# Optimization experiments

Measured on AMD Instinct MI355X. Metric: run time of the kernel, lower is better.

Reference implementation:

```python
import jax, jax.numpy as jnp
import numpy as np

N, E, F_IN, H, L, G, NH, HD, C = 50000, 640000, 64, 128, 3, 64, 8, 16, 2


def setup_inputs() -> dict:
    key = jax.random.key(0)
    k = jax.random.split(key, 12)
    s = 0.02
    return {
        "x": jax.random.normal(k[0], (N, F_IN), jnp.float32),
        "edge_index": jax.random.randint(k[1], (2, E), 0, N),
        "batch_idx": jnp.sort(jax.random.randint(k[2], (N,), 0, G)),
        "emb_w": jax.random.normal(k[3], (H, F_IN), jnp.float32) * s,
        "emb_b": jnp.zeros((H,), jnp.float32),
        "gcn_w": jax.random.normal(k[4], (L, H, H), jnp.float32) * s,
        "gcn_b": jnp.zeros((L, H), jnp.float32),
        "lstm_w_ih": jax.random.normal(k[5], (4 * H, H), jnp.float32) * s,
        "lstm_w_hh": jax.random.normal(k[6], (4 * H, H), jnp.float32) * s,
        "lstm_b_ih": jnp.zeros((4 * H,), jnp.float32),
        "lstm_b_hh": jnp.zeros((4 * H,), jnp.float32),
        "attn_in_w": jax.random.normal(k[7], (3 * H, H), jnp.float32) * s,
        "attn_in_b": jnp.zeros((3 * H,), jnp.float32),
        "attn_out_w": jax.random.normal(k[8], (H, H), jnp.float32) * s,
        "attn_out_b": jnp.zeros((H,), jnp.float32),
        "cls_w1": jax.random.normal(k[9], (H // 2, H), jnp.float32) * s,
        "cls_b1": jnp.zeros((H // 2,), jnp.float32),
        "cls_w2": jax.random.normal(k[10], (C, H // 2), jnp.float32) * s,
        "cls_b2": jnp.zeros((C,), jnp.float32),
    }


def reference(x, edge_index, batch_idx, emb_w, emb_b, gcn_w, gcn_b,
              lstm_w_ih, lstm_w_hh, lstm_b_ih, lstm_b_hh,
              attn_in_w, attn_in_b, attn_out_w, attn_out_b,
              cls_w1, cls_b1, cls_w2, cls_b2):
    src, dst = edge_index[0], edge_index[1]
    # GCN symmetric norm with self-loops (PyG gcn_norm): deg includes the self loop
    deg = jax.ops.segment_sum(jnp.ones((E,), x.dtype), dst, num_segments=N) + 1.0
    dis = jax.lax.rsqrt(deg)                      # deg^{-1/2}, deg >= 1
    norm = dis[src] * dis[dst]                    # [E]
    self_norm = dis * dis                         # [N], self-loop weight

    h = x @ emb_w.T + emb_b                       # node embedding [N, H]
    for l in range(L):
        hw = h @ gcn_w[l].T                       # linear transform [N, H]
        agg = jax.ops.segment_sum(hw[src] * norm[:, None], dst, num_segments=N)
        agg = agg + hw * self_norm[:, None]       # self-loop contribution
        h = jax.nn.relu(agg + gcn_b[l])

    # global mean pool per graph
    sums = jax.ops.segment_sum(h, batch_idx, num_segments=G)
    counts = jax.ops.segment_sum(jnp.ones((N,), h.dtype), batch_idx, num_segments=G)
    ge = sums / jnp.maximum(counts, 1.0)[:, None]  # [G, H]

    # LSTM with seq_len=1, h0=c0=0 (W_hh term vanishes); gate order i,f,g,o
    gates = ge @ lstm_w_ih.T + lstm_b_ih + lstm_b_hh
    i, f, g, o = jnp.split(gates, 4, axis=-1)
    c = jax.nn.sigmoid(i) * jnp.tanh(g)
    hs = jax.nn.sigmoid(o) * jnp.tanh(c)           # [G, H]

    # MultiheadAttention, seq_len=1 self-attention
    q, kk, v = jnp.split(hs @ attn_in_w.T + attn_in_b, 3, axis=-1)
    qh = q.reshape(G, NH, HD)
    kh = kk.reshape(G, NH, HD)
    vh = v.reshape(G, NH, HD)
    scores = jnp.einsum('bhd,bhd->bh', qh, kh) / jnp.sqrt(jnp.asarray(HD, hs.dtype))
    attn = jax.nn.softmax(scores[..., None], axis=-1)[..., 0]  # single key -> all ones
    ctx = (attn[..., None] * vh).reshape(G, H)
    fe = ctx @ attn_out_w.T + attn_out_b           # attended_out.mean(dim=1) with S=1

    # classifier (dropout is identity at inference)
    z = jax.nn.relu(fe @ cls_w1.T + cls_b1)
    return z @ cls_w2.T + cls_b2
```

## Files before the change

### kernel.cpp

```cpp
#include <hip/hip_runtime.h>
#include <math.h>

#define N_NODES 50000
#define N_EDGES 640000
#define F_INDIM 64
#define HDIM 128
#define NLAYERS 3
#define NGRAPH 64
#define NCLS 2
#define SCAN_BLOCKS ((N_NODES + 255) / 256)
#define POOL_SPLIT 8
#define NTILES (N_NODES / 16)

typedef __attribute__((ext_vector_type(8))) short bf16x8;
typedef __attribute__((ext_vector_type(4))) float f32x4;

__device__ __forceinline__ float bf_lo(unsigned v) { return __uint_as_float(v << 16); }
__device__ __forceinline__ float bf_hi(unsigned v) { return __uint_as_float(v & 0xffff0000u); }
__device__ __forceinline__ unsigned short f2bf(float f) {
    unsigned b = __float_as_uint(f);
    return (unsigned short)((b + 0x7fffu + ((b >> 16) & 1u)) >> 16);
}


__global__ __launch_bounds__(256) void k_init(int* cnt) {
    int i = blockIdx.x * 256 + threadIdx.x;
    if (i < N_NODES) cnt[i] = 0;
}

__global__ __launch_bounds__(256) void k_rank(const int* __restrict__ dst,
                                              int* __restrict__ cnt,
                                              int* __restrict__ rank) {
    int e = blockIdx.x * 256 + threadIdx.x;
    if (e < N_EDGES) rank[e] = atomicAdd(&cnt[dst[e]], 1);
}

__global__ __launch_bounds__(256) void k_scan1(const int* __restrict__ hist,
                                               int* __restrict__ row_start,
                                               int* __restrict__ partials,
                                               float* __restrict__ dis) {
    __shared__ int buf[256];
    int i = blockIdx.x * 256 + threadIdx.x;
    int v = (i < N_NODES) ? hist[i] : 0;
    if (i < N_NODES) dis[i] = rsqrtf((float)v + 1.0f);
    buf[threadIdx.x] = v;
    __syncthreads();
#pragma unroll
    for (int off = 1; off < 256; off <<= 1) {
        int t = (threadIdx.x >= off) ? buf[threadIdx.x - off] : 0;
        __syncthreads();
        buf[threadIdx.x] += t;
        __syncthreads();
    }
    if (i < N_NODES) row_start[i] = buf[threadIdx.x] - v;
    if (threadIdx.x == 255) partials[blockIdx.x] = buf[255];
}

__global__ __launch_bounds__(256) void k_scan2(int* __restrict__ partials) {
    __shared__ int buf[256];
    int v = (threadIdx.x < SCAN_BLOCKS) ? partials[threadIdx.x] : 0;
    buf[threadIdx.x] = v;
    __syncthreads();
#pragma unroll
    for (int off = 1; off < 256; off <<= 1) {
        int t = (threadIdx.x >= off) ? buf[threadIdx.x - off] : 0;
        __syncthreads();
        buf[threadIdx.x] += t;
        __syncthreads();
    }
    if (threadIdx.x < SCAN_BLOCKS) partials[threadIdx.x] = buf[threadIdx.x] - v;
}

__global__ __launch_bounds__(256) void k_scan3(int* __restrict__ row_start,
                                               const int* __restrict__ partials) {
    int i = blockIdx.x * 256 + threadIdx.x;
    if (i < N_NODES) row_start[i] += partials[blockIdx.x];
    if (i == 0) row_start[N_NODES] = N_EDGES;
}

#define PLACE_BLOCKS ((N_EDGES + 255) / 256)
#define CVT_Q1 (N_NODES * F_INDIM / 4)
#define CVT_Q2 (CVT_Q1 + HDIM * F_INDIM / 4)
#define CVT_Q3 (CVT_Q2 + NLAYERS * HDIM * HDIM / 4)
#define CVT_BLOCKS ((CVT_Q3 + 255) / 256)
#define ZERO_N (NGRAPH * HDIM + NGRAPH)
#define ZERO_BLOCKS ((ZERO_N + 255) / 256)

__global__ __launch_bounds__(256) void k_prep(const int* __restrict__ src,
                                              const int* __restrict__ dst,
                                              const int* __restrict__ rank,
                                              const float* __restrict__ dis,
                                              const int* __restrict__ row_start,
                                              uint2* __restrict__ csr,
                                              const float* __restrict__ x,
                                              const float* __restrict__ emb_w,
                                              const float* __restrict__ gcn_w,
                                              unsigned short* __restrict__ dst0,
                                              float* __restrict__ pool_counts) {
    int b = blockIdx.x;
    if (b < PLACE_BLOCKS) {
        int e = b * 256 + threadIdx.x;
        if (e >= N_EDGES) return;
        int s = src[e], d = dst[e];
        uint2 rec;
        rec.x = (unsigned)s;
        rec.y = __float_as_uint(dis[s] * dis[d]);
        csr[row_start[d] + rank[e]] = rec;
    } else if (b < PLACE_BLOCKS + CVT_BLOCKS) {
        int i = (b - PLACE_BLOCKS) * 256 + threadIdx.x;
        if (i >= CVT_Q3) return;
        const float* s;
        int off;
        if (i < CVT_Q1)      { s = x;     off = i; }
        else if (i < CVT_Q2) { s = emb_w; off = i - CVT_Q1; }
        else                 { s = gcn_w; off = i - CVT_Q2; }
        float4 v = *(const float4*)&s[off * 4];
        unsigned r0 = (unsigned)f2bf(v.x) | ((unsigned)f2bf(v.y) << 16);
        unsigned r1 = (unsigned)f2bf(v.z) | ((unsigned)f2bf(v.w) << 16);
        *(uint2*)&dst0[i * 4] = make_uint2(r0, r1);
    } else {
        int i = (b - PLACE_BLOCKS - CVT_BLOCKS) * 256 + threadIdx.x;
        if (i < ZERO_N) pool_counts[i] = 0.f;
    }
}


template<int K>
__global__ __launch_bounds__(256) void k_mm(const unsigned short* __restrict__ A,
                                            const unsigned short* __restrict__ W,
                                            const float* __restrict__ bias,
                                            unsigned short* __restrict__ C) {
    constexpr int KS = K / 32;
    int lane = threadIdx.x & 63;
    int lg = lane >> 4, lr = lane & 15;
    int cb = (threadIdx.x >> 6) * 32;
    int tile0 = blockIdx.x * 4;

    bf16x8 wf[2][KS];
#pragma unroll
    for (int ct = 0; ct < 2; ++ct)
#pragma unroll
        for (int ks = 0; ks < KS; ++ks)
            wf[ct][ks] = *(const bf16x8*)&W[(size_t)(cb + ct * 16 + lr) * K + ks * 32 + lg * 8];

    float b0 = bias ? bias[cb + lr] : 0.f;
    float b1 = bias ? bias[cb + 16 + lr] : 0.f;

    int ntile = NTILES - tile0; if (ntile > 4) ntile = 4;
    for (int t = 0; t < ntile; ++t) {
        int rb = (tile0 + t) * 16;
        f32x4 acc0 = {0.f, 0.f, 0.f, 0.f}, acc1 = {0.f, 0.f, 0.f, 0.f};
#pragma unroll
        for (int ks = 0; ks < KS; ++ks) {
            bf16x8 af = *(const bf16x8*)&A[(size_t)(rb + lr) * K + ks * 32 + lg * 8];
            acc0 = __builtin_amdgcn_mfma_f32_16x16x32_bf16(af, wf[0][ks], acc0, 0, 0, 0);
            acc1 = __builtin_amdgcn_mfma_f32_16x16x32_bf16(af, wf[1][ks], acc1, 0, 0, 0);
        }
        int row = rb + lg * 4;
#pragma unroll
        for (int j = 0; j < 4; ++j) {
            C[(size_t)(row + j) * HDIM + cb + lr]      = f2bf(acc0[j] + b0);
            C[(size_t)(row + j) * HDIM + cb + 16 + lr] = f2bf(acc1[j] + b1);
        }
    }
}


__global__ __launch_bounds__(256) void k_gather(const unsigned short* __restrict__ hw,
                                                const int* __restrict__ row_start,
                                                const uint2* __restrict__ csr,
                                                const float* __restrict__ dis,
                                                const float* __restrict__ bias,
                                                unsigned short* __restrict__ hout) {
    int n = blockIdx.x * 4 + (threadIdx.x >> 6);
    int lane = threadIdx.x & 63;
    int half = lane >> 5;
    int cl = lane & 31;
    int beg = row_start[n], end = row_start[n + 1];
    float a0 = 0.f, a1 = 0.f, a2 = 0.f, a3 = 0.f;
    for (int e = beg; e < end; e += 16) {
        unsigned sidx[8]; float w[8]; uint2 v[8];
#pragma unroll
        for (int u = 0; u < 8; ++u) {
            int me = e + 2 * u + half;
            uint2 rec = csr[min(me, end - 1)];
            sidx[u] = rec.x;
            w[u] = (me < end) ? __uint_as_float(rec.y) : 0.f;
        }
#pragma unroll
        for (int u = 0; u < 8; ++u)
            v[u] = *(const uint2*)&hw[(size_t)sidx[u] * HDIM + cl * 4];
#pragma unroll
        for (int u = 0; u < 8; ++u) {
            a0 += w[u] * bf_lo(v[u].x);
            a1 += w[u] * bf_hi(v[u].x);
            a2 += w[u] * bf_lo(v[u].y);
            a3 += w[u] * bf_hi(v[u].y);
        }
    }
    a0 += __shfl_xor(a0, 32); a1 += __shfl_xor(a1, 32);
    a2 += __shfl_xor(a2, 32); a3 += __shfl_xor(a3, 32);
    if (half == 0) {
        float dn = dis[n], sn = dn * dn;
        uint2 vs = *(const uint2*)&hw[(size_t)n * HDIM + cl * 4];
        a0 += sn * bf_lo(vs.x); a1 += sn * bf_hi(vs.x);
        a2 += sn * bf_lo(vs.y); a3 += sn * bf_hi(vs.y);
        float4 b = *(const float4*)&bias[cl * 4];
        a0 = fmaxf(a0 + b.x, 0.f); a1 = fmaxf(a1 + b.y, 0.f);
        a2 = fmaxf(a2 + b.z, 0.f); a3 = fmaxf(a3 + b.w, 0.f);
        uint2 r;
        r.x = (unsigned)f2bf(a0) | ((unsigned)f2bf(a1) << 16);
        r.y = (unsigned)f2bf(a2) | ((unsigned)f2bf(a3) << 16);
        *(uint2*)&hout[(size_t)n * HDIM + cl * 4] = r;
    }
}


__global__ __launch_bounds__(256) void k_pool(const unsigned short* __restrict__ h,
                                              const int* __restrict__ batch,
                                              float* __restrict__ pool,
                                              float* __restrict__ counts) {
    int g  = blockIdx.x >> 3;
    int sp = blockIdx.x & 7;
    int s, e;
    {
        int lo = 0, hi = N_NODES;
        while (lo < hi) { int mid = (lo + hi) >> 1; if (batch[mid] < g) lo = mid + 1; else hi = mid; }
        s = lo;
        lo = s; hi = N_NODES;
        while (lo < hi) { int mid = (lo + hi) >> 1; if (batch[mid] < g + 1) lo = mid + 1; else hi = mid; }
        e = lo;
    }
    int len = e - s;
    int chunk = (len + POOL_SPLIT - 1) / POOL_SPLIT;
    int ss = s + sp * chunk;
    int ee = min(ss + chunk, e);
    int cp = threadIdx.x & 63;
    int r  = threadIdx.x >> 6;
    float a0 = 0.f, a1 = 0.f;
    for (int n = ss + r; n < ee; n += 4) {
        unsigned v = *(const unsigned*)&h[(size_t)n * HDIM + cp * 2];
        a0 += bf_lo(v);
        a1 += bf_hi(v);
    }
    __shared__ float red0[4][64], red1[4][64];
    red0[r][cp] = a0; red1[r][cp] = a1;
    __syncthreads();
    if (r == 0) {
#pragma unroll
        for (int j = 1; j < 4; ++j) { a0 += red0[j][cp]; a1 += red1[j][cp]; }
        atomicAdd(&pool[g * HDIM + cp * 2], a0);
        atomicAdd(&pool[g * HDIM + cp * 2 + 1], a1);
    }
    if (threadIdx.x == 0 && ee > ss) atomicAdd(&counts[g], (float)(ee - ss));
}


__global__ __launch_bounds__(128) void k_tail(const float* __restrict__ pool,
                                              const float* __restrict__ counts,
                                              const float* __restrict__ w_ih,
                                              const float* __restrict__ b_ih,
                                              const float* __restrict__ b_hh,
                                              const float* __restrict__ attn_in_w,
                                              const float* __restrict__ attn_in_b,
                                              const float* __restrict__ attn_out_w,
                                              const float* __restrict__ attn_out_b,
                                              const float* __restrict__ w1,
                                              const float* __restrict__ b1,
                                              const float* __restrict__ w2,
                                              const float* __restrict__ b2,
                                              float* __restrict__ out) {
    __shared__ float ge[128], hsr[128], vv[128], fe[128], zz[64];
    int g = blockIdx.x, t = threadIdx.x;
    float cnt = fmaxf(counts[g], 1.0f);
    ge[t] = pool[g * HDIM + t] / cnt;
    __syncthreads();
    float gi = 0.f, gg = 0.f, go = 0.f;
    for (int k = 0; k < 128; ++k) {
        float xv = ge[k];
        gi += xv * w_ih[t * HDIM + k];
        gg += xv * w_ih[(256 + t) * HDIM + k];
        go += xv * w_ih[(384 + t) * HDIM + k];
    }
    gi += b_ih[t] + b_hh[t];
    gg += b_ih[256 + t] + b_hh[256 + t];
    go += b_ih[384 + t] + b_hh[384 + t];
    float cc = (1.f / (1.f + expf(-gi))) * tanhf(gg);
    float hv = (1.f / (1.f + expf(-go))) * tanhf(cc);
    hsr[t] = hv;
    __syncthreads();
    float va = attn_in_b[256 + t];
    for (int k = 0; k < 128; ++k) va += hsr[k] * attn_in_w[(256 + t) * HDIM + k];
    vv[t] = va;
    __syncthreads();
    float fv = attn_out_b[t];
    for (int k = 0; k < 128; ++k) fv += vv[k] * attn_out_w[t * HDIM + k];
    fe[t] = fv;
    __syncthreads();
    if (t < 64) {
        float zv = b1[t];
        for (int k = 0; k < 128; ++k) zv += fe[k] * w1[t * HDIM + k];
        zz[t] = fmaxf(zv, 0.f);
    }
    __syncthreads();
    if (t < NCLS) {
        float ov = b2[t];
        for (int k = 0; k < 64; ++k) ov += zz[k] * w2[t * 64 + k];
        out[g * NCLS + t] = ov;
    }
}


extern "C" void kernel_launch(void* const* d_in, const int* in_sizes, int n_in,
                              void* d_out, int out_size, void* d_ws, size_t ws_size,
                              hipStream_t stream) {
    const float* x          = (const float*)d_in[0];
    const int*   edge_index = (const int*)d_in[1];
    const int*   batch      = (const int*)d_in[2];
    const float* emb_w      = (const float*)d_in[3];
    const float* emb_b      = (const float*)d_in[4];
    const float* gcn_w      = (const float*)d_in[5];
    const float* gcn_b      = (const float*)d_in[6];
    const float* w_ih       = (const float*)d_in[7];
    const float* b_ih       = (const float*)d_in[9];
    const float* b_hh       = (const float*)d_in[10];
    const float* attn_in_w  = (const float*)d_in[11];
    const float* attn_in_b  = (const float*)d_in[12];
    const float* attn_out_w = (const float*)d_in[13];
    const float* attn_out_b = (const float*)d_in[14];
    const float* w1         = (const float*)d_in[15];
    const float* b1         = (const float*)d_in[16];
    const float* w2         = (const float*)d_in[17];
    const float* b2         = (const float*)d_in[18];
    float* out = (float*)d_out;

    int*   iws = (int*)d_ws;
    float* fws = (float*)d_ws;
    int*   cnt       = iws;
    float* dis       = fws + N_NODES;
    int*   row_start = iws + 2 * N_NODES;
    int*   rank      = iws + 3 * N_NODES + 4;
    uint2* csr       = (uint2*)(iws + 3 * N_NODES + 4 + N_EDGES);
    unsigned short* bws   = (unsigned short*)(iws + 3 * N_NODES + 4 + N_EDGES + 2 * N_EDGES);
    unsigned short* x_bf  = bws;
    unsigned short* we_bf = x_bf + (size_t)N_NODES * F_INDIM;
    unsigned short* wg_bf = we_bf + HDIM * F_INDIM;
    unsigned short* hA    = wg_bf + NLAYERS * HDIM * HDIM;
    unsigned short* hB    = hA + (size_t)N_NODES * HDIM;
    float* pool     = (float*)(hB + (size_t)N_NODES * HDIM);
    float* counts   = pool + NGRAPH * HDIM;
    int*   partials = (int*)(counts + NGRAPH);

    const int* src = edge_index;
    const int* dst = edge_index + N_EDGES;

    k_init<<<196, 256, 0, stream>>>(cnt);
    k_rank<<<(N_EDGES + 255) / 256, 256, 0, stream>>>(dst, cnt, rank);
    k_scan1<<<SCAN_BLOCKS, 256, 0, stream>>>(cnt, row_start, partials, dis);
    k_scan2<<<1, 256, 0, stream>>>(partials);
    k_scan3<<<SCAN_BLOCKS, 256, 0, stream>>>(row_start, partials);

    k_prep<<<PLACE_BLOCKS + CVT_BLOCKS + ZERO_BLOCKS, 256, 0, stream>>>(
        src, dst, rank, dis, row_start, csr, x, emb_w, gcn_w, x_bf, pool);

    int mm_grid = (NTILES + 3) / 4;
    k_mm<F_INDIM><<<mm_grid, 256, 0, stream>>>(x_bf, we_bf, emb_b, hA);
    for (int l = 0; l < NLAYERS; ++l) {
        k_mm<HDIM><<<mm_grid, 256, 0, stream>>>(hA, wg_bf + l * HDIM * HDIM, nullptr, hB);
        k_gather<<<N_NODES / 4, 256, 0, stream>>>(hB, row_start, csr, dis,
                                                  gcn_b + l * HDIM, hA);
    }
    k_pool<<<NGRAPH * POOL_SPLIT, 256, 0, stream>>>(hA, batch, pool, counts);
    k_tail<<<NGRAPH, 128, 0, stream>>>(pool, counts, w_ih, b_ih, b_hh,
                                       attn_in_w, attn_in_b, attn_out_w, attn_out_b,
                                       w1, b1, w2, b2, out);
}
```

Measured before the change: 261.1 us.

## Build CSR via bucketed two-pass sort and drop per-edge norm weights

```diff
diff --git a/kernel.cpp b/kernel.cpp
--- a/kernel.cpp
+++ b/kernel.cpp
@@ -8,9 +8,12 @@
 #define NLAYERS 3
 #define NGRAPH 64
 #define NCLS 2
-#define SCAN_BLOCKS ((N_NODES + 255) / 256)
 #define POOL_SPLIT 8
 #define NTILES (N_NODES / 16)
+
+#define NBUCK 64
+#define BNODES 782
+#define BSTRIDE 12288
 
 typedef __attribute__((ext_vector_type(8))) short bf16x8;
 typedef __attribute__((ext_vector_type(4))) float f32x4;
@@ -23,62 +26,133 @@
 }
 
 
-__global__ __launch_bounds__(256) void k_init(int* cnt) {
-    int i = blockIdx.x * 256 + threadIdx.x;
-    if (i < N_NODES) cnt[i] = 0;
-}
-
-__global__ __launch_bounds__(256) void k_rank(const int* __restrict__ dst,
-                                              int* __restrict__ cnt,
-                                              int* __restrict__ rank) {
-    int e = blockIdx.x * 256 + threadIdx.x;
-    if (e < N_EDGES) rank[e] = atomicAdd(&cnt[dst[e]], 1);
-}
-
-__global__ __launch_bounds__(256) void k_scan1(const int* __restrict__ hist,
+__global__ __launch_bounds__(256) void k_init(int* bcursor) {
+    if (threadIdx.x < NBUCK) bcursor[threadIdx.x] = 0;
+}
+
+__global__ __launch_bounds__(256) void k_bscatter(const int* __restrict__ src,
+                                                  const int* __restrict__ dst,
+                                                  int* __restrict__ bcursor,
+                                                  uint2* __restrict__ stage) {
+    __shared__ uint2 q[NBUCK][32];
+    __shared__ int qn[NBUCK];
+    __shared__ int qh[NBUCK];
+    int tid = threadIdx.x;
+    if (tid < NBUCK) { qn[tid] = 0; qh[tid] = 0; }
+    __syncthreads();
+    for (int base = blockIdx.x * 256; base < N_EDGES; base += gridDim.x * 256) {
+        int e = base + tid;
+        if (e < N_EDGES) {
+            uint2 rec = make_uint2((unsigned)src[e], (unsigned)dst[e]);
+            int b = (int)rec.y / BNODES;
+            int pos = atomicAdd(&qn[b], 1);
+            if (pos < 24) {
+                q[b][(qh[b] + pos) & 31] = rec;
+            } else {
+                atomicSub(&qn[b], 1);
+                int gp = atomicAdd(&bcursor[b], 1);
+                stage[(size_t)b * BSTRIDE + gp] = rec;
+            }
+        }
+        __syncthreads();
+        if (tid < NBUCK) {
+            int bb = tid;
+            while (qn[bb] >= 8) {
+                int gp = atomicAdd(&bcursor[bb], 8);
+                int h = qh[bb];
+                uint2* dp = &stage[(size_t)bb * BSTRIDE + gp];
+#pragma unroll
+                for (int j = 0; j < 8; ++j) dp[j] = q[bb][(h + j) & 31];
+                qh[bb] = (h + 8) & 31;
+                qn[bb] -= 8;
+            }
+        }
+        __syncthreads();
+    }
+    if (tid < NBUCK) {
+        int bb = tid, cnt = qn[bb];
+        if (cnt > 0) {
+            int gp = atomicAdd(&bcursor[bb], cnt);
+            int h = qh[bb];
+            for (int j = 0; j < cnt; ++j)
+                stage[(size_t)bb * BSTRIDE + gp + j] = q[bb][(h + j) & 31];
+        }
+    }
+}
+
+__global__ __launch_bounds__(64) void k_bscan(const int* __restrict__ bcursor,
+                                              int* __restrict__ bbase,
+                                              int* __restrict__ row_start) {
+    __shared__ int buf[64];
+    int t = threadIdx.x;
+    int v = bcursor[t];
+    buf[t] = v;
+    __syncthreads();
+#pragma unroll
+    for (int off = 1; off < 64; off <<= 1) {
+        int x = (t >= off) ? buf[t - off] : 0;
+        __syncthreads();
+        buf[t] += x;
+        __syncthreads();
+    }
+    bbase[t] = buf[t] - v;
+    if (t == 0) row_start[N_NODES] = N_EDGES;
+}
+
+__global__ __launch_bounds__(256) void k_bsort(const uint2* __restrict__ stage,
+                                               const int* __restrict__ bcursor,
+                                               const int* __restrict__ bbase,
+                                               int* __restrict__ csr_src,
                                                int* __restrict__ row_start,
-                                               int* __restrict__ partials,
                                                float* __restrict__ dis) {
+    __shared__ int ndeg[BNODES];
+    __shared__ int noff[BNODES];
     __shared__ int buf[256];
-    int i = blockIdx.x * 256 + threadIdx.x;
-    int v = (i < N_NODES) ? hist[i] : 0;
-    if (i < N_NODES) dis[i] = rsqrtf((float)v + 1.0f);
-    buf[threadIdx.x] = v;
-    __syncthreads();
-#pragma unroll
-    for (int off = 1; off < 256; off <<= 1) {
-        int t = (threadIdx.x >= off) ? buf[threadIdx.x - off] : 0;
-        __syncthreads();
-        buf[threadIdx.x] += t;
-        __syncthreads();
-    }
-    if (i < N_NODES) row_start[i] = buf[threadIdx.x] - v;
-    if (threadIdx.x == 255) partials[blockIdx.x] = buf[255];
-}
-
-__global__ __launch_bounds__(256) void k_scan2(int* __restrict__ partials) {
-    __shared__ int buf[256];
-    int v = (threadIdx.x < SCAN_BLOCKS) ? partials[threadIdx.x] : 0;
-    buf[threadIdx.x] = v;
-    __syncthreads();
-#pragma unroll
-    for (int off = 1; off < 256; off <<= 1) {
-        int t = (threadIdx.x >= off) ? buf[threadIdx.x - off] : 0;
-        __syncthreads();
-        buf[threadIdx.x] += t;
-        __syncthreads();
-    }
-    if (threadIdx.x < SCAN_BLOCKS) partials[threadIdx.x] = buf[threadIdx.x] - v;
-}
-
-__global__ __launch_bounds__(256) void k_scan3(int* __restrict__ row_start,
-                                               const int* __restrict__ partials) {
-    int i = blockIdx.x * 256 + threadIdx.x;
-    if (i < N_NODES) row_start[i] += partials[blockIdx.x];
-    if (i == 0) row_start[N_NODES] = N_EDGES;
-}
-
-#define PLACE_BLOCKS ((N_EDGES + 255) / 256)
+    __shared__ int carry;
+    int b = blockIdx.x, tid = threadIdx.x;
+    int cnt = bcursor[b], base = bbase[b];
+    const uint2* seg = &stage[(size_t)b * BSTRIDE];
+    for (int i = tid; i < BNODES; i += 256) ndeg[i] = 0;
+    if (tid == 0) carry = 0;
+    __syncthreads();
+    for (int i = tid; i < cnt; i += 256)
+        atomicAdd(&ndeg[(int)seg[i].y - b * BNODES], 1);
+    __syncthreads();
+    for (int cb = 0; cb < BNODES; cb += 256) {
+        int idx = cb + tid;
+        int v = (idx < BNODES) ? ndeg[idx] : 0;
+        buf[tid] = v;
+        __syncthreads();
+#pragma unroll
+        for (int off = 1; off < 256; off <<= 1) {
+            int x = (tid >= off) ? buf[tid - off] : 0;
+            __syncthreads();
+            buf[tid] += x;
+            __syncthreads();
+        }
+        if (idx < BNODES) noff[idx] = carry + buf[tid] - v;
+        __syncthreads();
+        if (tid == 255) carry += buf[255];
+        __syncthreads();
+    }
+    for (int i = tid; i < BNODES; i += 256) {
+        int node = b * BNODES + i;
+        if (node < N_NODES) {
+            row_start[node] = base + noff[i];
+            dis[node] = rsqrtf((float)ndeg[i] + 1.0f);
+        }
+    }
+    __syncthreads();
+    for (int i = tid; i < BNODES; i += 256) ndeg[i] = 0;
+    __syncthreads();
+    for (int i = tid; i < cnt; i += 256) {
+        uint2 r = seg[i];
+        int d = (int)r.y - b * BNODES;
+        int rk = atomicAdd(&ndeg[d], 1);
+        csr_src[base + noff[d] + rk] = (int)r.x;
+    }
+}
+
 #define CVT_Q1 (N_NODES * F_INDIM / 4)
 #define CVT_Q2 (CVT_Q1 + HDIM * F_INDIM / 4)
 #define CVT_Q3 (CVT_Q2 + NLAYERS * HDIM * HDIM / 4)
@@ -86,28 +160,14 @@
 #define ZERO_N (NGRAPH * HDIM + NGRAPH)
 #define ZERO_BLOCKS ((ZERO_N + 255) / 256)
 
-__global__ __launch_bounds__(256) void k_prep(const int* __restrict__ src,
-                                              const int* __restrict__ dst,
-                                              const int* __restrict__ rank,
-                                              const float* __restrict__ dis,
-                                              const int* __restrict__ row_start,
-                                              uint2* __restrict__ csr,
-                                              const float* __restrict__ x,
+__global__ __launch_bounds__(256) void k_prep(const float* __restrict__ x,
                                               const float* __restrict__ emb_w,
                                               const float* __restrict__ gcn_w,
                                               unsigned short* __restrict__ dst0,
                                               float* __restrict__ pool_counts) {
     int b = blockIdx.x;
-    if (b < PLACE_BLOCKS) {
-        int e = b * 256 + threadIdx.x;
-        if (e >= N_EDGES) return;
-        int s = src[e], d = dst[e];
-        uint2 rec;
-        rec.x = (unsigned)s;
-        rec.y = __float_as_uint(dis[s] * dis[d]);
-        csr[row_start[d] + rank[e]] = rec;
-    } else if (b < PLACE_BLOCKS + CVT_BLOCKS) {
-        int i = (b - PLACE_BLOCKS) * 256 + threadIdx.x;
+    if (b < CVT_BLOCKS) {
+        int i = b * 256 + threadIdx.x;
         if (i >= CVT_Q3) return;
         const float* s;
         int off;
@@ -119,7 +179,7 @@
         unsigned r1 = (unsigned)f2bf(v.z) | ((unsigned)f2bf(v.w) << 16);
         *(uint2*)&dst0[i * 4] = make_uint2(r0, r1);
     } else {
-        int i = (b - PLACE_BLOCKS - CVT_BLOCKS) * 256 + threadIdx.x;
+        int i = (b - CVT_BLOCKS) * 256 + threadIdx.x;
         if (i < ZERO_N) pool_counts[i] = 0.f;
     }
 }
@@ -168,7 +228,7 @@
 
 __global__ __launch_bounds__(256) void k_gather(const unsigned short* __restrict__ hw,
                                                 const int* __restrict__ row_start,
-                                                const uint2* __restrict__ csr,
+                                                const int* __restrict__ csr_src,
                                                 const float* __restrict__ dis,
                                                 const float* __restrict__ bias,
                                                 unsigned short* __restrict__ hout) {
@@ -179,35 +239,37 @@
     int beg = row_start[n], end = row_start[n + 1];
     float a0 = 0.f, a1 = 0.f, a2 = 0.f, a3 = 0.f;
     for (int e = beg; e < end; e += 16) {
-        unsigned sidx[8]; float w[8]; uint2 v[8];
+        int sidx[8]; float ds[8]; uint2 v[8];
 #pragma unroll
         for (int u = 0; u < 8; ++u) {
             int me = e + 2 * u + half;
-            uint2 rec = csr[min(me, end - 1)];
-            sidx[u] = rec.x;
-            w[u] = (me < end) ? __uint_as_float(rec.y) : 0.f;
-        }
+            sidx[u] = csr_src[min(me, end - 1)];
+            ds[u] = (me < end) ? 1.f : 0.f;
+        }
+#pragma unroll
+        for (int u = 0; u < 8; ++u)
+            ds[u] *= dis[sidx[u]];
 #pragma unroll
         for (int u = 0; u < 8; ++u)
             v[u] = *(const uint2*)&hw[(size_t)sidx[u] * HDIM + cl * 4];
 #pragma unroll
         for (int u = 0; u < 8; ++u) {
-            a0 += w[u] * bf_lo(v[u].x);
-            a1 += w[u] * bf_hi(v[u].x);
-            a2 += w[u] * bf_lo(v[u].y);
-            a3 += w[u] * bf_hi(v[u].y);
+            a0 += ds[u] * bf_lo(v[u].x);
+            a1 += ds[u] * bf_hi(v[u].x);
+            a2 += ds[u] * bf_lo(v[u].y);
+            a3 += ds[u] * bf_hi(v[u].y);
         }
     }
     a0 += __shfl_xor(a0, 32); a1 += __shfl_xor(a1, 32);
     a2 += __shfl_xor(a2, 32); a3 += __shfl_xor(a3, 32);
     if (half == 0) {
-        float dn = dis[n], sn = dn * dn;
+        float dn = dis[n];
         uint2 vs = *(const uint2*)&hw[(size_t)n * HDIM + cl * 4];
-        a0 += sn * bf_lo(vs.x); a1 += sn * bf_hi(vs.x);
-        a2 += sn * bf_lo(vs.y); a3 += sn * bf_hi(vs.y);
+        a0 += dn * bf_lo(vs.x); a1 += dn * bf_hi(vs.x);
+        a2 += dn * bf_lo(vs.y); a3 += dn * bf_hi(vs.y);
         float4 b = *(const float4*)&bias[cl * 4];
-        a0 = fmaxf(a0 + b.x, 0.f); a1 = fmaxf(a1 + b.y, 0.f);
-        a2 = fmaxf(a2 + b.z, 0.f); a3 = fmaxf(a3 + b.w, 0.f);
+        a0 = fmaxf(dn * a0 + b.x, 0.f); a1 = fmaxf(dn * a1 + b.y, 0.f);
+        a2 = fmaxf(dn * a2 + b.z, 0.f); a3 = fmaxf(dn * a3 + b.w, 0.f);
         uint2 r;
         r.x = (unsigned)f2bf(a0) | ((unsigned)f2bf(a1) << 16);
         r.y = (unsigned)f2bf(a2) | ((unsigned)f2bf(a3) << 16);
@@ -336,12 +398,13 @@
 
     int*   iws = (int*)d_ws;
     float* fws = (float*)d_ws;
-    int*   cnt       = iws;
-    float* dis       = fws + N_NODES;
-    int*   row_start = iws + 2 * N_NODES;
-    int*   rank      = iws + 3 * N_NODES + 4;
-    uint2* csr       = (uint2*)(iws + 3 * N_NODES + 4 + N_EDGES);
-    unsigned short* bws   = (unsigned short*)(iws + 3 * N_NODES + 4 + N_EDGES + 2 * N_EDGES);
+    int*   bcursor   = iws;
+    int*   bbase     = iws + 64;
+    int*   row_start = iws + 128;
+    float* dis       = fws + 50132;
+    int*   csr_src   = iws + 100136;
+    uint2* stage     = (uint2*)(iws + 740136);
+    unsigned short* bws   = (unsigned short*)(iws + 740136 + 2 * NBUCK * BSTRIDE);
     unsigned short* x_bf  = bws;
     unsigned short* we_bf = x_bf + (size_t)N_NODES * F_INDIM;
     unsigned short* wg_bf = we_bf + HDIM * F_INDIM;
@@ -349,25 +412,22 @@
     unsigned short* hB    = hA + (size_t)N_NODES * HDIM;
     float* pool     = (float*)(hB + (size_t)N_NODES * HDIM);
     float* counts   = pool + NGRAPH * HDIM;
-    int*   partials = (int*)(counts + NGRAPH);
 
     const int* src = edge_index;
     const int* dst = edge_index + N_EDGES;
 
-    k_init<<<196, 256, 0, stream>>>(cnt);
-    k_rank<<<(N_EDGES + 255) / 256, 256, 0, stream>>>(dst, cnt, rank);
-    k_scan1<<<SCAN_BLOCKS, 256, 0, stream>>>(cnt, row_start, partials, dis);
-    k_scan2<<<1, 256, 0, stream>>>(partials);
-    k_scan3<<<SCAN_BLOCKS, 256, 0, stream>>>(row_start, partials);
-
-    k_prep<<<PLACE_BLOCKS + CVT_BLOCKS + ZERO_BLOCKS, 256, 0, stream>>>(
-        src, dst, rank, dis, row_start, csr, x, emb_w, gcn_w, x_bf, pool);
+    k_init<<<1, 256, 0, stream>>>(bcursor);
+    k_bscatter<<<128, 256, 0, stream>>>(src, dst, bcursor, stage);
+    k_bscan<<<1, 64, 0, stream>>>(bcursor, bbase, row_start);
+    k_bsort<<<NBUCK, 256, 0, stream>>>(stage, bcursor, bbase, csr_src, row_start, dis);
+
+    k_prep<<<CVT_BLOCKS + ZERO_BLOCKS, 256, 0, stream>>>(x, emb_w, gcn_w, x_bf, pool);
 
     int mm_grid = (NTILES + 3) / 4;
     k_mm<F_INDIM><<<mm_grid, 256, 0, stream>>>(x_bf, we_bf, emb_b, hA);
     for (int l = 0; l < NLAYERS; ++l) {
         k_mm<HDIM><<<mm_grid, 256, 0, stream>>>(hA, wg_bf + l * HDIM * HDIM, nullptr, hB);
-        k_gather<<<N_NODES / 4, 256, 0, stream>>>(hB, row_start, csr, dis,
+        k_gather<<<N_NODES / 4, 256, 0, stream>>>(hB, row_start, csr_src, dis,
                                                   gcn_b + l * HDIM, hA);
     }
     k_pool<<<NGRAPH * POOL_SPLIT, 256, 0, stream>>>(hA, batch, pool, counts);
```

After: 289.5 us. 10.9% more time.
